# Kernel tuning notes

Measured on AMD Instinct MI355X. Metric: run time of the kernel, lower is better.

The kernel has to match this reference:

```python
import jax, jax.numpy as jnp
from jax import lax
import numpy as np

T, B, D, H = 512, 256, 128, 256
SHIFT = 0.0


def setup_inputs() -> dict:
    key = jax.random.key(0)
    ks = jax.random.split(key, 11)
    s_in = 1.0 / np.sqrt(D + H)
    s_cl = 1.0 / np.sqrt(H)
    return {
        "inputs": jax.random.normal(ks[0], (T, B, D), dtype=jnp.float32),
        "Wf": jax.random.normal(ks[1], (H, D + H), dtype=jnp.float32) * s_in,
        "bf": jax.random.normal(ks[2], (H,), dtype=jnp.float32) * s_in,
        "Wi": jax.random.normal(ks[3], (H, D + H), dtype=jnp.float32) * s_in,
        "bi": jax.random.normal(ks[4], (H,), dtype=jnp.float32) * s_in,
        "Wg": jax.random.normal(ks[5], (H, D + H), dtype=jnp.float32) * s_in,
        "bg": jax.random.normal(ks[6], (H,), dtype=jnp.float32) * s_in,
        "Wo": jax.random.normal(ks[7], (H, D + H), dtype=jnp.float32) * s_in,
        "bo": jax.random.normal(ks[8], (H,), dtype=jnp.float32) * s_in,
        "Wc": jax.random.normal(ks[9], (1, H), dtype=jnp.float32) * s_cl,
        "bc": jax.random.normal(ks[10], (1,), dtype=jnp.float32) * s_cl,
    }


def reference(inputs, Wf, bf, Wi, bi, Wg, bg, Wo, bo, Wc, bc):
    # Fuse the four gate linears into one GEMM per step: [4H, D+H]
    W = jnp.concatenate([Wf, Wi, Wg, Wo], axis=0)
    b = jnp.concatenate([bf, bi, bg, bo], axis=0)
    h = W.shape[0] // 4
    batch = inputs.shape[1]

    def step(carry, x):
        hx, cx = carry
        combined = jnp.concatenate([x, hx], axis=1)      # [B, D+H]
        z = combined @ W.T + b                            # [B, 4H]
        f = jax.nn.sigmoid(z[:, 0 * h:1 * h])
        i = jax.nn.sigmoid(z[:, 1 * h:2 * h])
        g = jnp.tanh(z[:, 2 * h:3 * h])
        o = jax.nn.sigmoid(z[:, 3 * h:4 * h])
        cx = f * cx + i * g
        hx = o * jnp.tanh(cx)
        return (hx, cx), hx

    h0 = jnp.zeros((batch, h), dtype=inputs.dtype)
    c0 = jnp.zeros((batch, h), dtype=inputs.dtype)
    (hx, cx), hs = lax.scan(step, (h0, c0), inputs)       # hs: [T, B, H]

    logits = hs @ Wc.T + bc                               # [T, B, 1]
    probs = jax.nn.sigmoid(logits + SHIFT)
    return (jnp.concatenate([probs, 1.0 - probs], axis=-1), hx, cx)
```

## Files before the change

### kernel.cpp

```cpp
#include <hip/hip_runtime.h>
#include <hip/hip_bf16.h>


#define T_STEPS 512
#define BATCH   256
#define DIN     128
#define HID     256
#define KDIM    384
#define LDK     392
#define GRIDN   256
#define NPOLL   96

typedef __attribute__((ext_vector_type(8))) short short8;
typedef __attribute__((ext_vector_type(4))) short short4v;
typedef __attribute__((ext_vector_type(4))) float f32x4;

__device__ __forceinline__ unsigned short f2bf(float f) {
    unsigned u = __float_as_uint(f);
    unsigned r = (u + 0x7FFFu + ((u >> 16) & 1u)) >> 16;
    return (unsigned short)r;
}
__device__ __forceinline__ float bf2f(unsigned short s) {
    return __uint_as_float(((unsigned)s) << 16);
}
__device__ __forceinline__ float sigmoid_f(float x) {
    return 1.f / (1.f + __expf(-x));
}
__device__ __forceinline__ float tanh_f(float x) {
    float e = __expf(2.f * x);
    return 1.f - 2.f / (e + 1.f);
}
__device__ __forceinline__ void poll_load_sc0(const unsigned int* p, uint4& a,
                                              uint4& b, uint4& c, uint4& d) {
    asm volatile(
        "global_load_dwordx4 %0, %4, off sc0\n\t"
        "global_load_dwordx4 %1, %4, off offset:16 sc0\n\t"
        "global_load_dwordx4 %2, %4, off offset:32 sc0\n\t"
        "global_load_dwordx4 %3, %4, off offset:48 sc0\n\t"
        "s_waitcnt vmcnt(0)"
        : "=&v"(a), "=&v"(b), "=&v"(c), "=&v"(d) : "v"(p) : "memory");
}
__device__ __forceinline__ void poll_load_sc1(const unsigned int* p, uint4& a,
                                              uint4& b, uint4& c, uint4& d) {
    asm volatile(
        "global_load_dwordx4 %0, %4, off sc1\n\t"
        "global_load_dwordx4 %1, %4, off offset:16 sc1\n\t"
        "global_load_dwordx4 %2, %4, off offset:32 sc1\n\t"
        "global_load_dwordx4 %3, %4, off offset:48 sc1\n\t"
        "s_waitcnt vmcnt(0)"
        : "=&v"(a), "=&v"(b), "=&v"(c), "=&v"(d) : "v"(p) : "memory");
}
__device__ __forceinline__ void store_plain_u32(unsigned int* p, unsigned int v) {
    asm volatile("global_store_dword %0, %1, off" :: "v"(p), "v"(v) : "memory");
}
__device__ __forceinline__ void store_sc1_u32(unsigned int* p, unsigned int v) {
    asm volatile("global_store_dword %0, %1, off sc1" :: "v"(p), "v"(v) : "memory");
}
__device__ __forceinline__ unsigned pack2bf(unsigned lo, unsigned hi) {
    return (hi & 0xFFFF0000u) | (lo >> 16);
}
__device__ __forceinline__ bool tags_ok(const uint4& a, const uint4& b,
                                        const uint4& c, const uint4& d,
                                        unsigned tag) {
    return ((a.x ^ tag) & 0xFFFFu) == 0 && ((a.y ^ tag) & 0xFFFFu) == 0 &&
           ((a.z ^ tag) & 0xFFFFu) == 0 && ((a.w ^ tag) & 0xFFFFu) == 0 &&
           ((b.x ^ tag) & 0xFFFFu) == 0 && ((b.y ^ tag) & 0xFFFFu) == 0 &&
           ((b.z ^ tag) & 0xFFFFu) == 0 && ((b.w ^ tag) & 0xFFFFu) == 0 &&
           ((c.x ^ tag) & 0xFFFFu) == 0 && ((c.y ^ tag) & 0xFFFFu) == 0 &&
           ((c.z ^ tag) & 0xFFFFu) == 0 && ((c.w ^ tag) & 0xFFFFu) == 0 &&
           ((d.x ^ tag) & 0xFFFFu) == 0 && ((d.y ^ tag) & 0xFFFFu) == 0 &&
           ((d.z ^ tag) & 0xFFFFu) == 0 && ((d.w ^ tag) & 0xFFFFu) == 0;
}

__global__ __launch_bounds__(256) void pack_w(
    const float* __restrict__ Wf, const float* __restrict__ Wi,
    const float* __restrict__ Wg, const float* __restrict__ Wo,
    unsigned short* __restrict__ Wp) {
    int idx = blockIdx.x * 256 + threadIdx.x;
    int n = idx / KDIM;
    int k = idx - n * KDIM;
    int g = n >> 8, j = n & 255;
    const float* s = (g == 0) ? Wf : (g == 1) ? Wi : (g == 2) ? Wg : Wo;
    Wp[idx] = f2bf(s[j * KDIM + k]);
}

__global__ __launch_bounds__(256) void pack_b(
    const float* __restrict__ bf, const float* __restrict__ bi,
    const float* __restrict__ bg, const float* __restrict__ bo,
    float* __restrict__ bp) {
    int n = blockIdx.x * 256 + threadIdx.x;
    int g = n >> 8, j = n & 255;
    const float* s = (g == 0) ? bf : (g == 1) ? bi : (g == 2) ? bg : bo;
    bp[n] = s[j];
}

__global__ __launch_bounds__(256) void init_k(unsigned int* __restrict__ hxp) {
    int tid = blockIdx.x * 256 + threadIdx.x;
    hxp[tid] = 0u;
    hxp[65536 + tid] = 0u;
    hxp[131072 + tid] = 0u;
    hxp[196608 + tid] = 0u;
}

__global__ __launch_bounds__(256, 1) void lstm_persist(
    const float* __restrict__ X,
    const unsigned short* __restrict__ W,
    const float* __restrict__ bias,
    unsigned int* __restrict__ hxp,
    unsigned short* __restrict__ hist,
    float* __restrict__ out) {
    __shared__ __align__(16) unsigned short W_s[64 * LDK];
    __shared__ __align__(16) unsigned short comb_s[16 * LDK];
    __shared__ __align__(16) float z_s[4 * 272];
    __shared__ int fastok_s;

    const int tid = threadIdx.x;
    const int bg = blockIdx.x & 15, jg = blockIdx.x >> 4;
    const int b0 = bg * 16, j0 = jg * 16;
    const int wave = tid >> 6, lane = tid & 63;
    const int l16 = lane & 15, quad = lane >> 4;
    const int bi = tid >> 4, jj = tid & 15;
    const int b = b0 + bi, j = j0 + jj;

#pragma unroll
    for (int c = 0; c < 12; ++c) {
        int q = c * 256 + tid;
        int row = q / 48, c8 = q - row * 48;
        int g = row >> 4, jr = row & 15;
        short8 v = *(const short8*)(W + ((g * 256 + j0 + jr) * KDIM + c8 * 8));
        *(short8*)(&W_s[row * LDK + c8 * 8]) = v;
    }
    const float bs0 = bias[0 * HID + j];
    const float bs1 = bias[1 * HID + j];
    const float bs2 = bias[2 * HID + j];
    const float bs3 = bias[3 * HID + j];
    if (tid == 0) fastok_s = 1;

    float c_reg = 0.f;
    float h_final = 0.f;

    const unsigned short* arow = &comb_s[l16 * LDK + quad * 8];
    const unsigned short* brow = &W_s[(wave * 16 + l16) * LDK + quad * 8];
    const int hrow = tid >> 4, hc = tid & 15;
    const int xr0 = tid >> 5, xc4 = tid & 31, xr1 = (tid + 256) >> 5;

    const float* xb = X + b0 * DIN;
    float4 xv0 = *(const float4*)(xb + xr0 * DIN + xc4 * 4);
    float4 xv1 = *(const float4*)(xb + xr1 * DIN + xc4 * 4);

    __syncthreads();

    for (int k = 0; k < T_STEPS; ++k) {
        const unsigned tag = (unsigned)k;
        const unsigned int* fb =
            hxp + (k & 1) * 65536 + (b0 + hrow) * HID + hc * 16;
        const unsigned int* sb = fb + 131072;
        uint4 a, bq, cq, d;
        const int usefast = fastok_s;

        {
            short4v r;
            r.x = (short)f2bf(xv0.x); r.y = (short)f2bf(xv0.y);
            r.z = (short)f2bf(xv0.z); r.w = (short)f2bf(xv0.w);
            *(short4v*)(&comb_s[xr0 * LDK + xc4 * 4]) = r;
            r.x = (short)f2bf(xv1.x); r.y = (short)f2bf(xv1.y);
            r.z = (short)f2bf(xv1.z); r.w = (short)f2bf(xv1.w);
            *(short4v*)(&comb_s[xr1 * LDK + xc4 * 4]) = r;
        }

        if (usefast) {
            int tries = NPOLL;
            bool ok = false;
            for (;;) {
                poll_load_sc0(fb, a, bq, cq, d);
                if (tags_ok(a, bq, cq, d, tag)) { ok = true; break; }
                if (--tries == 0) break;
            }
            if (!ok) {
                fastok_s = 0;
                for (;;) {
                    poll_load_sc1(sb, a, bq, cq, d);
                    if (tags_ok(a, bq, cq, d, tag)) break;
                    __builtin_amdgcn_s_sleep(1);
                }
            }
        } else {
            for (;;) {
                poll_load_sc1(sb, a, bq, cq, d);
                if (tags_ok(a, bq, cq, d, tag)) break;
                __builtin_amdgcn_s_sleep(1);
            }
        }

        {
            uint4 p0, p1;
            p0.x = pack2bf(a.x, a.y);   p0.y = pack2bf(a.z, a.w);
            p0.z = pack2bf(bq.x, bq.y); p0.w = pack2bf(bq.z, bq.w);
            p1.x = pack2bf(cq.x, cq.y); p1.y = pack2bf(cq.z, cq.w);
            p1.z = pack2bf(d.x, d.y);   p1.w = pack2bf(d.z, d.w);
            *(uint4*)(&comb_s[hrow * LDK + DIN + hc * 16]) = p0;
            *(uint4*)(&comb_s[hrow * LDK + DIN + hc * 16 + 8]) = p1;
        }
        __syncthreads();

        f32x4 acc0 = {0.f, 0.f, 0.f, 0.f}, acc1 = {0.f, 0.f, 0.f, 0.f};
#pragma unroll
        for (int kt = 0; kt < 6; ++kt) {
            short8 a0 = *(const short8*)(arow + (2 * kt) * 32);
            short8 b0v = *(const short8*)(brow + (2 * kt) * 32);
            short8 a1 = *(const short8*)(arow + (2 * kt + 1) * 32);
            short8 b1v = *(const short8*)(brow + (2 * kt + 1) * 32);
            acc0 = __builtin_amdgcn_mfma_f32_16x16x32_bf16(a0, b0v, acc0, 0, 0, 0);
            acc1 = __builtin_amdgcn_mfma_f32_16x16x32_bf16(a1, b1v, acc1, 0, 0, 0);
        }
#pragma unroll
        for (int r = 0; r < 4; ++r)
            z_s[wave * 272 + (quad * 4 + r) * 17 + l16] = acc0[r] + acc1[r];
        __syncthreads();

        float zf = z_s[0 * 272 + bi * 17 + jj] + bs0;
        float zi = z_s[1 * 272 + bi * 17 + jj] + bs1;
        float zg = z_s[2 * 272 + bi * 17 + jj] + bs2;
        float zo = z_s[3 * 272 + bi * 17 + jj] + bs3;
        float fg = sigmoid_f(zf);
        float ig = sigmoid_f(zi);
        float gg = tanh_f(zg);
        float og = sigmoid_f(zo);
        c_reg = fg * c_reg + ig * gg;
        float hval = og * tanh_f(c_reg);
        unsigned short hb = f2bf(hval);
        unsigned int hword = ((unsigned)hb << 16) | (unsigned)(k + 1);
        unsigned int* fdst = hxp + ((k + 1) & 1) * 65536 + b * HID + j;
        store_plain_u32(fdst, hword);
        store_sc1_u32(fdst + 131072, hword);
        hist[(size_t)k * BATCH * HID + b * HID + j] = hb;
        if (k + 1 < T_STEPS) {
            const float* xn = X + (size_t)(k + 1) * BATCH * DIN + b0 * DIN;
            xv0 = *(const float4*)(xn + xr0 * DIN + xc4 * 4);
            xv1 = *(const float4*)(xn + xr1 * DIN + xc4 * 4);
        } else {
            h_final = hval;
        }
    }

    out[T_STEPS * BATCH * 2 + b * HID + j] = h_final;
    out[T_STEPS * BATCH * 2 + BATCH * HID + b * HID + j] = c_reg;
}

__global__ __launch_bounds__(256) void probs_k(
    const unsigned short* __restrict__ hist, const float* __restrict__ Wc,
    const float* __restrict__ bc, float* __restrict__ out) {
    const int wave = threadIdx.x >> 6, lane = threadIdx.x & 63;
    const size_t row = (size_t)blockIdx.x * 4 + wave;
    const unsigned short* h = hist + row * HID;
    short4v hv = *(const short4v*)(h + lane * 4);
    const float4 wv = *(const float4*)(Wc + lane * 4);
    float p = bf2f((unsigned short)hv.x) * wv.x + bf2f((unsigned short)hv.y) * wv.y +
              bf2f((unsigned short)hv.z) * wv.z + bf2f((unsigned short)hv.w) * wv.w;
#pragma unroll
    for (int off = 32; off >= 1; off >>= 1) p += __shfl_down(p, off);
    if (lane == 0) {
        float prob = 1.f / (1.f + __expf(-(p + bc[0])));
        out[row * 2]     = prob;
        out[row * 2 + 1] = 1.f - prob;
    }
}

extern "C" void kernel_launch(void* const* d_in, const int* in_sizes, int n_in,
                              void* d_out, int out_size, void* d_ws, size_t ws_size,
                              hipStream_t stream) {
    const float* X  = (const float*)d_in[0];
    const float* Wf = (const float*)d_in[1];
    const float* bfp= (const float*)d_in[2];
    const float* Wi = (const float*)d_in[3];
    const float* bip= (const float*)d_in[4];
    const float* Wg = (const float*)d_in[5];
    const float* bgp= (const float*)d_in[6];
    const float* Wo = (const float*)d_in[7];
    const float* bop= (const float*)d_in[8];
    const float* Wc = (const float*)d_in[9];
    const float* bc = (const float*)d_in[10];
    float* out = (float*)d_out;

    char* ws = (char*)d_ws;
    unsigned short* Wpack = (unsigned short*)(ws);
    float* bias = (float*)(ws + 786432);
    unsigned int* hxp = (unsigned int*)(ws + 790528);
    unsigned short* hist = (unsigned short*)(ws + 1839104);

    pack_w<<<1536, 256, 0, stream>>>(Wf, Wi, Wg, Wo, Wpack);
    pack_b<<<4, 256, 0, stream>>>(bfp, bip, bgp, bop, bias);
    init_k<<<256, 256, 0, stream>>>(hxp);

    void* kargs[6] = {(void*)&X, (void*)&Wpack, (void*)&bias,
                      (void*)&hxp, (void*)&hist, (void*)&out};
    (void)hipLaunchCooperativeKernel((const void*)lstm_persist, dim3(GRIDN),
                                     dim3(256), kargs, 0, stream);

    probs_k<<<32768, 256, 0, stream>>>(hist, Wc, bc, out);
}
```

Before: 1.183 ms.

## Hold gate weights in registers and double-buffer x prefetch across unrolled steps

Moves each wave's bf16 weight fragments from LDS into twelve short8 registers, so the per-step MFMA loop only reads the activation tile from shared memory. The time loop is unrolled by two with separate x registers, letting the next-next step's input be prefetched two steps ahead. It also replaces __syncthreads with a lighter lgkmcnt-wait plus s_barrier. A large dummy LDS pad keeps one block per CU, and the extra registers raise VGPR pressure.

```diff
diff --git a/kernel.cpp b/kernel.cpp
--- a/kernel.cpp
+++ b/kernel.cpp
@@ -29,6 +29,10 @@
 __device__ __forceinline__ float tanh_f(float x) {
     float e = __expf(2.f * x);
     return 1.f - 2.f / (e + 1.f);
+}
+__device__ __forceinline__ void barrier_lds() {
+    asm volatile("s_waitcnt lgkmcnt(0)" ::: "memory");
+    __builtin_amdgcn_s_barrier();
 }
 __device__ __forceinline__ void poll_load_sc0(const unsigned int* p, uint4& a,
                                               uint4& b, uint4& c, uint4& d) {
@@ -102,6 +106,99 @@
     hxp[196608 + tid] = 0u;
 }
 
+#define LSTM_STEP(kk, xc0, xc1)                                               \
+    {                                                                         \
+        const unsigned tag = (unsigned)(kk);                                  \
+                               \
+        {                                                                     \
+            short4v r;                                                        \
+            r.x = (short)f2bf(xc0.x); r.y = (short)f2bf(xc0.y);               \
+            r.z = (short)f2bf(xc0.z); r.w = (short)f2bf(xc0.w);               \
+            *(short4v*)(&comb_s[xr0 * LDK + xc4 * 4]) = r;                    \
+            r.x = (short)f2bf(xc1.x); r.y = (short)f2bf(xc1.y);               \
+            r.z = (short)f2bf(xc1.z); r.w = (short)f2bf(xc1.w);               \
+            *(short4v*)(&comb_s[xr1 * LDK + xc4 * 4]) = r;                    \
+        }                                                                     \
+        const unsigned int* fb =                                              \
+            hxp + ((kk) & 1) * 65536 + (b0 + hrow) * HID + hc * 16;           \
+        const unsigned int* sb = fb + 131072;                                 \
+        uint4 a, bq, cq, d;                                                   \
+        const int usefast = fastok_s;                                         \
+        if (usefast) {                                                        \
+            int tries = NPOLL;                                                \
+            bool ok = false;                                                  \
+            for (;;) {                                                        \
+                poll_load_sc0(fb, a, bq, cq, d);                              \
+                if (tags_ok(a, bq, cq, d, tag)) { ok = true; break; }         \
+                if (--tries == 0) break;                                      \
+            }                                                                 \
+            if (!ok) {                                                        \
+                fastok_s = 0;                                                 \
+                for (;;) {                                                    \
+                    poll_load_sc1(sb, a, bq, cq, d);                          \
+                    if (tags_ok(a, bq, cq, d, tag)) break;                    \
+                    __builtin_amdgcn_s_sleep(1);                              \
+                }                                                             \
+            }                                                                 \
+        } else {                                                              \
+            for (;;) {                                                        \
+                poll_load_sc1(sb, a, bq, cq, d);                              \
+                if (tags_ok(a, bq, cq, d, tag)) break;                        \
+                __builtin_amdgcn_s_sleep(1);                                  \
+            }                                                                 \
+        }                                                                     \
+                         \
+        {                                                                     \
+            uint4 p0, p1;                                                     \
+            p0.x = pack2bf(a.x, a.y);   p0.y = pack2bf(a.z, a.w);             \
+            p0.z = pack2bf(bq.x, bq.y); p0.w = pack2bf(bq.z, bq.w);           \
+            p1.x = pack2bf(cq.x, cq.y); p1.y = pack2bf(cq.z, cq.w);           \
+            p1.z = pack2bf(d.x, d.y);   p1.w = pack2bf(d.z, d.w);             \
+            *(uint4*)(&comb_s[hrow * LDK + DIN + hc * 16]) = p0;              \
+            *(uint4*)(&comb_s[hrow * LDK + DIN + hc * 16 + 8]) = p1;          \
+        }                                                                     \
+        \
+        if ((kk) + 2 < T_STEPS) {                                             \
+            const float* xn = X + (size_t)((kk) + 2) * BATCH * DIN + b0 * DIN;\
+            xc0 = *(const float4*)(xn + xr0 * DIN + xc4 * 4);                 \
+            xc1 = *(const float4*)(xn + xr1 * DIN + xc4 * 4);                 \
+        }                                                                     \
+        barrier_lds();                                                        \
+                              \
+        f32x4 acc0 = {0.f, 0.f, 0.f, 0.f}, acc1 = {0.f, 0.f, 0.f, 0.f};       \
+        _Pragma("unroll")                                                     \
+        for (int kt = 0; kt < 6; ++kt) {                                      \
+            short8 a0 = *(const short8*)(arow + (2 * kt) * 32);               \
+            short8 a1 = *(const short8*)(arow + (2 * kt + 1) * 32);           \
+            acc0 = __builtin_amdgcn_mfma_f32_16x16x32_bf16(a0, wf[2 * kt],    \
+                                                           acc0, 0, 0, 0);    \
+            acc1 = __builtin_amdgcn_mfma_f32_16x16x32_bf16(a1, wf[2 * kt + 1],\
+                                                           acc1, 0, 0, 0);    \
+        }                                                                     \
+        _Pragma("unroll")                                                     \
+        for (int r = 0; r < 4; ++r)                                           \
+            z_s[wave * 272 + (quad * 4 + r) * 17 + l16] = acc0[r] + acc1[r];  \
+        barrier_lds();                                                        \
+                      \
+        float zf = z_s[0 * 272 + bi * 17 + jj] + bs0;                         \
+        float zi = z_s[1 * 272 + bi * 17 + jj] + bs1;                         \
+        float zg = z_s[2 * 272 + bi * 17 + jj] + bs2;                         \
+        float zo = z_s[3 * 272 + bi * 17 + jj] + bs3;                         \
+        float fg = sigmoid_f(zf);                                             \
+        float ig = sigmoid_f(zi);                                             \
+        float gg = tanh_f(zg);                                                \
+        float og = sigmoid_f(zo);                                             \
+        c_reg = fg * c_reg + ig * gg;                                         \
+        float hval = og * tanh_f(c_reg);                                      \
+        unsigned short hb = f2bf(hval);                                       \
+        unsigned int hword = ((unsigned)hb << 16) | (unsigned)((kk) + 1);     \
+        unsigned int* fdst = hxp + (((kk) + 1) & 1) * 65536 + b * HID + j;    \
+        store_plain_u32(fdst, hword);                                         \
+        store_sc1_u32(fdst + 131072, hword);                                  \
+        hist[(size_t)(kk) * BATCH * HID + b * HID + j] = hb;                  \
+        if ((kk) == T_STEPS - 1) { h_final = hval; }                          \
+    }
+
 __global__ __launch_bounds__(256, 1) void lstm_persist(
     const float* __restrict__ X,
     const unsigned short* __restrict__ W,
@@ -109,9 +206,9 @@
     unsigned int* __restrict__ hxp,
     unsigned short* __restrict__ hist,
     float* __restrict__ out) {
-    __shared__ __align__(16) unsigned short W_s[64 * LDK];
     __shared__ __align__(16) unsigned short comb_s[16 * LDK];
     __shared__ __align__(16) float z_s[4 * 272];
+    __shared__ char lds_pad[68000];
     __shared__ int fastok_s;
 
     const int tid = threadIdx.x;
@@ -122,125 +219,41 @@
     const int bi = tid >> 4, jj = tid & 15;
     const int b = b0 + bi, j = j0 + jj;
 
+    if (tid == 0) { fastok_s = 1; lds_pad[0] = (char)blockIdx.x; }
+    (void)lds_pad;
+
+    short8 wf[12];
+    {
+        const unsigned short* wbase =
+            W + (wave * 256 + j0 + l16) * KDIM + quad * 8;
 #pragma unroll
-    for (int c = 0; c < 12; ++c) {
-        int q = c * 256 + tid;
-        int row = q / 48, c8 = q - row * 48;
-        int g = row >> 4, jr = row & 15;
-        short8 v = *(const short8*)(W + ((g * 256 + j0 + jr) * KDIM + c8 * 8));
-        *(short8*)(&W_s[row * LDK + c8 * 8]) = v;
+        for (int kt = 0; kt < 12; ++kt)
+            wf[kt] = *(const short8*)(wbase + kt * 32);
     }
     const float bs0 = bias[0 * HID + j];
     const float bs1 = bias[1 * HID + j];
     const float bs2 = bias[2 * HID + j];
     const float bs3 = bias[3 * HID + j];
-    if (tid == 0) fastok_s = 1;
 
     float c_reg = 0.f;
     float h_final = 0.f;
 
     const unsigned short* arow = &comb_s[l16 * LDK + quad * 8];
-    const unsigned short* brow = &W_s[(wave * 16 + l16) * LDK + quad * 8];
     const int hrow = tid >> 4, hc = tid & 15;
     const int xr0 = tid >> 5, xc4 = tid & 31, xr1 = (tid + 256) >> 5;
 
-    const float* xb = X + b0 * DIN;
-    float4 xv0 = *(const float4*)(xb + xr0 * DIN + xc4 * 4);
-    float4 xv1 = *(const float4*)(xb + xr1 * DIN + xc4 * 4);
+    const float* xb0p = X + b0 * DIN;
+    const float* xb1p = X + (size_t)BATCH * DIN + b0 * DIN;
+    float4 xa0 = *(const float4*)(xb0p + xr0 * DIN + xc4 * 4);
+    float4 xa1 = *(const float4*)(xb0p + xr1 * DIN + xc4 * 4);
+    float4 xb0 = *(const float4*)(xb1p + xr0 * DIN + xc4 * 4);
+    float4 xb1 = *(const float4*)(xb1p + xr1 * DIN + xc4 * 4);
 
     __syncthreads();
 
-    for (int k = 0; k < T_STEPS; ++k) {
-        const unsigned tag = (unsigned)k;
-        const unsigned int* fb =
-            hxp + (k & 1) * 65536 + (b0 + hrow) * HID + hc * 16;
-        const unsigned int* sb = fb + 131072;
-        uint4 a, bq, cq, d;
-        const int usefast = fastok_s;
-
-        {
-            short4v r;
-            r.x = (short)f2bf(xv0.x); r.y = (short)f2bf(xv0.y);
-            r.z = (short)f2bf(xv0.z); r.w = (short)f2bf(xv0.w);
-            *(short4v*)(&comb_s[xr0 * LDK + xc4 * 4]) = r;
-            r.x = (short)f2bf(xv1.x); r.y = (short)f2bf(xv1.y);
-            r.z = (short)f2bf(xv1.z); r.w = (short)f2bf(xv1.w);
-            *(short4v*)(&comb_s[xr1 * LDK + xc4 * 4]) = r;
-        }
-
-        if (usefast) {
-            int tries = NPOLL;
-            bool ok = false;
-            for (;;) {
-                poll_load_sc0(fb, a, bq, cq, d);
-                if (tags_ok(a, bq, cq, d, tag)) { ok = true; break; }
-                if (--tries == 0) break;
-            }
-            if (!ok) {
-                fastok_s = 0;
-                for (;;) {
-                    poll_load_sc1(sb, a, bq, cq, d);
-                    if (tags_ok(a, bq, cq, d, tag)) break;
-                    __builtin_amdgcn_s_sleep(1);
-                }
-            }
-        } else {
-            for (;;) {
-                poll_load_sc1(sb, a, bq, cq, d);
-                if (tags_ok(a, bq, cq, d, tag)) break;
-                __builtin_amdgcn_s_sleep(1);
-            }
-        }
-
-        {
-            uint4 p0, p1;
-            p0.x = pack2bf(a.x, a.y);   p0.y = pack2bf(a.z, a.w);
-            p0.z = pack2bf(bq.x, bq.y); p0.w = pack2bf(bq.z, bq.w);
-            p1.x = pack2bf(cq.x, cq.y); p1.y = pack2bf(cq.z, cq.w);
-            p1.z = pack2bf(d.x, d.y);   p1.w = pack2bf(d.z, d.w);
-            *(uint4*)(&comb_s[hrow * LDK + DIN + hc * 16]) = p0;
-            *(uint4*)(&comb_s[hrow * LDK + DIN + hc * 16 + 8]) = p1;
-        }
-        __syncthreads();
-
-        f32x4 acc0 = {0.f, 0.f, 0.f, 0.f}, acc1 = {0.f, 0.f, 0.f, 0.f};
-#pragma unroll
-        for (int kt = 0; kt < 6; ++kt) {
-            short8 a0 = *(const short8*)(arow + (2 * kt) * 32);
-            short8 b0v = *(const short8*)(brow + (2 * kt) * 32);
-            short8 a1 = *(const short8*)(arow + (2 * kt + 1) * 32);
-            short8 b1v = *(const short8*)(brow + (2 * kt + 1) * 32);
-            acc0 = __builtin_amdgcn_mfma_f32_16x16x32_bf16(a0, b0v, acc0, 0, 0, 0);
-            acc1 = __builtin_amdgcn_mfma_f32_16x16x32_bf16(a1, b1v, acc1, 0, 0, 0);
-        }
-#pragma unroll
-        for (int r = 0; r < 4; ++r)
-            z_s[wave * 272 + (quad * 4 + r) * 17 + l16] = acc0[r] + acc1[r];
-        __syncthreads();
-
-        float zf = z_s[0 * 272 + bi * 17 + jj] + bs0;
-        float zi = z_s[1 * 272 + bi * 17 + jj] + bs1;
-        float zg = z_s[2 * 272 + bi * 17 + jj] + bs2;
-        float zo = z_s[3 * 272 + bi * 17 + jj] + bs3;
-        float fg = sigmoid_f(zf);
-        float ig = sigmoid_f(zi);
-        float gg = tanh_f(zg);
-        float og = sigmoid_f(zo);
-        c_reg = fg * c_reg + ig * gg;
-        float hval = og * tanh_f(c_reg);
-        unsigned short hb = f2bf(hval);
-        unsigned int hword = ((unsigned)hb << 16) | (unsigned)(k + 1);
-        unsigned int* fdst = hxp + ((k + 1) & 1) * 65536 + b * HID + j;
-        store_plain_u32(fdst, hword);
-        store_sc1_u32(fdst + 131072, hword);
-        hist[(size_t)k * BATCH * HID + b * HID + j] = hb;
-        if (k + 1 < T_STEPS) {
-            const float* xn = X + (size_t)(k + 1) * BATCH * DIN + b0 * DIN;
-            xv0 = *(const float4*)(xn + xr0 * DIN + xc4 * 4);
-            xv1 = *(const float4*)(xn + xr1 * DIN + xc4 * 4);
-        } else {
-            h_final = hval;
-        }
+    for (int k = 0; k < T_STEPS; k += 2) {
+        LSTM_STEP(k, xa0, xa1);
+        LSTM_STEP(k + 1, xb0, xb1);
     }
 
     out[T_STEPS * BATCH * 2 + b * HID + j] = h_final;
```

New measurement: 1.237 ms. 4.5% more time.
